# Optimization experiments

Hardware: AMD Instinct MI355X
Metric: run time of the kernel (lower is better)

The kernel has to match this reference:

```python
import jax, jax.numpy as jnp
import numpy as np

NUM_HEADS = 6
HEAD_SIZE = 64
N_EMBD = 384


def setup_inputs() -> dict:
    key = jax.random.key(0)
    ks = jax.random.split(key, 6)
    B, T, C = 4, 2048, N_EMBD
    D = NUM_HEADS * HEAD_SIZE  # 384
    x = jax.random.normal(ks[0], (B, T, C), dtype=jnp.float32)
    scale = 1.0 / np.sqrt(C)
    Wq = jax.random.normal(ks[1], (C, D), dtype=jnp.float32) * scale
    Wk = jax.random.normal(ks[2], (C, D), dtype=jnp.float32) * scale
    Wv = jax.random.normal(ks[3], (C, D), dtype=jnp.float32) * scale
    Wp = jax.random.normal(ks[4], (D, N_EMBD), dtype=jnp.float32) * scale
    bp = jnp.zeros((N_EMBD,), dtype=jnp.float32)
    return {"x": x, "Wq": Wq, "Wk": Wk, "Wv": Wv, "Wp": Wp, "bp": bp}


def reference(x, Wq, Wk, Wv, Wp, bp):
    B, T, C = x.shape
    H, Dh = NUM_HEADS, HEAD_SIZE
    # QKV projections (no bias), split into heads: [B, H, T, Dh]
    q = (x @ Wq).reshape(B, T, H, Dh).transpose(0, 2, 1, 3)
    k = (x @ Wk).reshape(B, T, H, Dh).transpose(0, 2, 1, 3)
    v = (x @ Wv).reshape(B, T, H, Dh).transpose(0, 2, 1, 3)
    # scaled dot-product scores [B, H, T, T]
    scores = jnp.einsum("bhqd,bhkd->bhqk", q, k) / jnp.sqrt(jnp.float32(Dh))
    causal = jnp.tril(jnp.ones((T, T), dtype=bool))
    scores = jnp.where(causal, scores, jnp.float32(-1e9))
    attn = jax.nn.softmax(scores, axis=-1)
    # dropout is identity at inference (Keras Dropout inactive outside training)
    out = jnp.einsum("bhqk,bhkd->bhqd", attn, v)
    out = out.transpose(0, 2, 1, 3).reshape(B, T, H * Dh)
    return out @ Wp + bp
```

## Files before the change

kernel.cpp:

```cpp
#include <hip/hip_runtime.h>
#include <hip/hip_bf16.h>

typedef __bf16 bf16x8 __attribute__((ext_vector_type(8)));
typedef float floatx4 __attribute__((ext_vector_type(4)));
typedef unsigned short us4 __attribute__((ext_vector_type(4)));
typedef unsigned short us8 __attribute__((ext_vector_type(8)));
typedef unsigned short ushort_t;

#define MFMA(a,b,c) __builtin_amdgcn_mfma_f32_16x16x32_bf16((a),(b),(c),0,0,0)


__device__ __forceinline__ ushort_t f2bf(float f){
  unsigned u = __builtin_bit_cast(unsigned, f);
  u = u + 0x7fffu + ((u>>16)&1u);
  return (ushort_t)(u>>16);
}

__device__ __forceinline__ us4 pack4(float4 a){
  us4 o;
  o[0]=f2bf(a.x); o[1]=f2bf(a.y); o[2]=f2bf(a.z); o[3]=f2bf(a.w);
  return o;
}

__device__ __forceinline__ us4 cvt4(floatx4 v){
  union { us4 s; __hip_bfloat162 h[2]; } u;
  float2 t;
  t.x=v[0]; t.y=v[1]; u.h[0]=__float22bfloat162_rn(t);
  t.x=v[2]; t.y=v[3]; u.h[1]=__float22bfloat162_rn(t);
  return u.s;
}

__global__ __launch_bounds__(256) void prep(
    const float* __restrict__ x,
    const float* __restrict__ w0, const float* __restrict__ w1,
    const float* __restrict__ w2, const float* __restrict__ w3,
    ushort_t* __restrict__ xb,
    ushort_t* __restrict__ wt_qkv, ushort_t* __restrict__ wt_p){
  __shared__ ushort_t tile[64][65];
  int bx = blockIdx.x;
  if (bx < 3072){
    int i = (bx*256 + threadIdx.x)*4;
    int row = i/384, col = i - row*384;
    float4 v = *(const float4*)(x + i);
    us4 o;
    o[0]=f2bf(v.x); o[1]=f2bf(v.y); o[2]=f2bf(v.z); o[3]=f2bf(v.w);
    *(us4*)(xb + ((row>>4)*48 + (col>>3))*128 + (row&15)*8 + (col&7)) = o;
    return;
  }
  int t6 = bx - 3072;
  int z = t6/36, rem = t6%36, by = rem/6, bxx = rem%6;
  const float* src; ushort_t* dst;
  if      (z==0){ src=w0; dst=wt_qkv;             }
  else if (z==1){ src=w1; dst=wt_qkv + 147456;    }
  else if (z==2){ src=w2; dst=wt_qkv + 2*147456;  }
  else          { src=w3; dst=wt_p;               }
  int r0 = by*64, c0 = bxx*64;
  int t = threadIdx.x, r = t>>2, cs = (t&3)*16;
  #pragma unroll
  for (int i=0;i<16;i++) tile[r][cs+i] = f2bf(src[(r0+r)*384 + c0+cs+i]);
  __syncthreads();
  int n = c0 + r, t16n = n>>4, rn = n&15;
  int k0 = r0 + cs;
  #pragma unroll
  for (int i=0;i<16;i++){
    int k = k0 + i;
    dst[(t16n*48 + (k>>3))*128 + rn*8 + (k&7)] = tile[cs+i][r];
  }
}

__global__ __launch_bounds__(64) void qkv_gemm(
    const ushort_t* __restrict__ x, const ushort_t* __restrict__ wt,
    ushort_t* __restrict__ qb, ushort_t* __restrict__ kb, ushort_t* __restrict__ vtb){
  int lane = threadIdx.x&63, l15 = lane&15, quad = lane>>4;
  int mb = blockIdx.x*64, mt = blockIdx.x*4;
  int z  = blockIdx.y/6;
  int nt16 = (blockIdx.y - z*6)*4;
  int n0 = nt16*16;
  const ushort_t* wbase = wt + z*147456;
  floatx4 acc[4][4];
  #pragma unroll
  for (int qs=0;qs<4;qs++)
    #pragma unroll
    for (int nt=0;nt<4;nt++) acc[qs][nt]=(floatx4){0,0,0,0};
  #pragma unroll
  for (int kt=0; kt<12; kt++){
    bf16x8 a[4], b[4];
    #pragma unroll
    for (int qs=0; qs<4; qs++)
      a[qs] = *(const bf16x8*)(x + ((mt+qs)*48 + kt*4+quad)*128 + l15*8);
    #pragma unroll
    for (int nt=0; nt<4; nt++)
      b[nt] = *(const bf16x8*)(wbase + ((nt16+nt)*48 + kt*4+quad)*128 + l15*8);
    #pragma unroll
    for (int qs=0; qs<4; qs++)
      #pragma unroll
      for (int nt=0; nt<4; nt++)
        acc[qs][nt] = MFMA(a[qs], b[nt], acc[qs][nt]);
  }
  int h = n0>>6;
  if (z == 2){
    #pragma unroll
    for (int qs=0; qs<4; qs++){
      int rbase = mb + qs*16 + quad*4;
      int b_ = rbase >> 11, rr = rbase & 2047;
      int ct = rr>>3, e0 = rr&7;
      #pragma unroll
      for (int nt=0; nt<4; nt++){
        float4 v; v.x=acc[qs][nt][0]; v.y=acc[qs][nt][1];
                  v.z=acc[qs][nt][2]; v.w=acc[qs][nt][3];
        *(us4*)(vtb + ((b_*6+h)*1024 + nt*256 + ct)*128 + l15*8 + e0) = pack4(v);
      }
    }
  } else {
    #pragma unroll
    for (int qs=0; qs<4; qs++){
      int rbase = mb + qs*16 + quad*4;
      int b_ = rbase>>11, rr = rbase&2047;
      int t16 = rr>>4, rlo = rr&15;
      #pragma unroll
      for (int nt=0; nt<4; nt++){
        int hc = nt*16 + l15;
        int base = ((b_*6+h)*1024 + t16*8 + (hc>>3))*128 + (hc&7);
        #pragma unroll
        for (int j=0; j<4; j++){
          float val = acc[qs][nt][j];
          if (z==0) val *= 0.18033688011112042f;
          ushort_t hv = f2bf(val);
          if (z==0) qb[base + (rlo+j)*8] = hv;
          else      kb[base + (rlo+j)*8] = hv;
        }
      }
    }
  }
}

__device__ __forceinline__ void subtile(
    const bf16x8 (&kf)[4][2], const bf16x8 (&vf)[4][2], bf16x8 ones,
    bf16x8 qf0, bf16x8 qf1,
    floatx4 (&o4)[4], floatx4& lsum,
    ushort_t* pwv, int qg, int kv0, bool diag, int l15, int quad){
  floatx4 s[4];
  #pragma unroll
  for (int nt=0; nt<4; nt++){
    floatx4 z = {0,0,0,0};
    z = MFMA(kf[nt][0], qf0, z);
    z = MFMA(kf[nt][1], qf1, z);
    s[nt] = z;
  }
  ushort_t* prow = pwv + l15*72;
  if (diag){
    #pragma unroll
    for (int nt=0; nt<4; nt++){
      floatx4 p;
      #pragma unroll
      for (int r=0;r<4;r++){
        int kvg = kv0 + nt*16 + quad*4 + r;
        float sv = (kvg > qg) ? -1e30f : s[nt][r];
        p[r] = exp2f(sv);
      }
      *(us4*)(prow + nt*16 + quad*4) = cvt4(p);
    }
  } else {
    #pragma unroll
    for (int nt=0; nt<4; nt++){
      floatx4 p;
      #pragma unroll
      for (int r=0;r<4;r++) p[r] = exp2f(s[nt][r]);
      *(us4*)(prow + nt*16 + quad*4) = cvt4(p);
    }
  }
  bf16x8 pa0 = *(const bf16x8*)(prow + quad*8);
  bf16x8 pa1 = *(const bf16x8*)(prow + 32 + quad*8);
  #pragma unroll
  for (int nt=0; nt<4; nt++){
    o4[nt] = MFMA(pa0, vf[nt][0], o4[nt]);
    o4[nt] = MFMA(pa1, vf[nt][1], o4[nt]);
  }
  lsum = MFMA(pa0, ones, lsum);
  lsum = MFMA(pa1, ones, lsum);
}

__global__ __launch_bounds__(256,2) void attn(
    const ushort_t* __restrict__ qb, const ushort_t* __restrict__ kb,
    const ushort_t* __restrict__ vtb, ushort_t* __restrict__ ob){
  __shared__ float smem[4608];
  int bx = blockIdx.x;
  int hb = bx % 24;
  int qi = bx / 24;
  int qt = 31 - qi;
  int h = hb % 6, b = hb / 6;
  int lane = threadIdx.x&63, w = threadIdx.x>>6, l15 = lane&15, quad = lane>>4;
  int q0 = qt*64;
  const ushort_t* qbase = qb  + (b*6+h)*131072;
  const ushort_t* kbase = kb  + (b*6+h)*131072;
  const ushort_t* vbase = vtb + (b*6+h)*131072;

  bf16x8 qf[4][2];
  #pragma unroll
  for (int qs=0; qs<4; qs++){
    const ushort_t* qp = qbase + ((qt*4+qs)*8 + quad)*128 + l15*8;
    qf[qs][0] = *(const bf16x8*)(qp);
    qf[qs][1] = *(const bf16x8*)(qp + 512);
  }
  union { us8 u; bf16x8 v; } onesu;
  #pragma unroll
  for (int i=0;i<8;i++) onesu.u[i] = 0x3F80;
  bf16x8 ones = onesu.v;

  floatx4 o[4][4];
  floatx4 lsum[4];
  #pragma unroll
  for (int qs=0;qs<4;qs++){
    lsum[qs] = (floatx4){0,0,0,0};
    #pragma unroll
    for (int i=0;i<4;i++) o[qs][i]=(floatx4){0,0,0,0};
  }

  ushort_t* pw = (ushort_t*)smem + w*1152;

  for (int kt=w; kt<=qt; kt+=4){
    int kv0 = kt*64;
    bf16x8 kf[4][2], vf[4][2];
    #pragma unroll
    for (int nt=0; nt<4; nt++){
      const ushort_t* kp = kbase + ((kt*4+nt)*8 + quad)*128 + l15*8;
      kf[nt][0] = *(const bf16x8*)(kp);
      kf[nt][1] = *(const bf16x8*)(kp + 512);
      const ushort_t* vp = vbase + (nt*256 + kt*8 + quad)*128 + l15*8;
      vf[nt][0] = *(const bf16x8*)(vp);
      vf[nt][1] = *(const bf16x8*)(vp + 512);
    }
    bool diag = (kt == qt);
    subtile(kf,vf,ones,qf[0][0],qf[0][1], o[0], lsum[0], pw, q0   +l15, kv0, diag, l15, quad);
    subtile(kf,vf,ones,qf[1][0],qf[1][1], o[1], lsum[1], pw, q0+16+l15, kv0, diag, l15, quad);
    subtile(kf,vf,ones,qf[2][0],qf[2][1], o[2], lsum[2], pw, q0+32+l15, kv0, diag, l15, quad);
    subtile(kf,vf,ones,qf[3][0],qf[3][1], o[3], lsum[3], pw, q0+48+l15, kv0, diag, l15, quad);
  }

  float* lsh = smem + 4352;
  if (l15==0){
    #pragma unroll
    for (int qs=0;qs<4;qs++)
      #pragma unroll
      for (int j=0;j<4;j++)
        lsh[w*64 + qs*16 + quad*4 + j] = lsum[qs][j];
  }

  #pragma unroll
  for (int qs=0; qs<4; qs++){
    __syncthreads();
    #pragma unroll
    for (int j=0;j<4;j++){
      int r16 = quad*4 + j;
      #pragma unroll
      for (int nt=0;nt<4;nt++)
        smem[w*1088 + r16*68 + nt*16 + l15] = o[qs][nt][j];
    }
    __syncthreads();
    #pragma unroll
    for (int jj=0;jj<4;jj++){
      int r16 = w*4 + jj;
      float l = lsh[qs*16+r16] + lsh[64+qs*16+r16]
              + lsh[128+qs*16+r16] + lsh[192+qs*16+r16];
      float acc = smem[r16*68+lane] + smem[1088 + r16*68+lane]
                + smem[2176 + r16*68+lane] + smem[3264 + r16*68+lane];
      ob[((b*128 + qt*4 + qs)*48 + h*8 + (lane>>3))*128 + r16*8 + (lane&7)]
          = f2bf(acc/l);
    }
  }
}

__global__ __launch_bounds__(64) void proj_gemm(
    const ushort_t* __restrict__ a, const ushort_t* __restrict__ wpt,
    const float* __restrict__ bp, float* __restrict__ out){
  int lane = threadIdx.x&63, l15 = lane&15, quad = lane>>4;
  int mb = blockIdx.x*64, mt = blockIdx.x*4;
  int nb = blockIdx.y*64, nt16 = blockIdx.y*4;
  floatx4 acc[4][4];
  #pragma unroll
  for (int qs=0;qs<4;qs++)
    #pragma unroll
    for (int nt=0;nt<4;nt++) acc[qs][nt]=(floatx4){0,0,0,0};
  #pragma unroll
  for (int kt=0; kt<12; kt++){
    bf16x8 av[4], bv[4];
    #pragma unroll
    for (int qs=0; qs<4; qs++)
      av[qs] = *(const bf16x8*)(a + ((mt+qs)*48 + kt*4+quad)*128 + l15*8);
    #pragma unroll
    for (int nt=0; nt<4; nt++)
      bv[nt] = *(const bf16x8*)(wpt + ((nt16+nt)*48 + kt*4+quad)*128 + l15*8);
    #pragma unroll
    for (int qs=0; qs<4; qs++)
      #pragma unroll
      for (int nt=0; nt<4; nt++)
        acc[qs][nt] = MFMA(av[qs], bv[nt], acc[qs][nt]);
  }
  #pragma unroll
  for (int qs=0; qs<4; qs++){
    #pragma unroll
    for (int nt=0; nt<4; nt++){
      int c = nb + nt*16 + l15;
      float bias = bp[c];
      #pragma unroll
      for (int j=0; j<4; j++){
        int r = mb + qs*16 + quad*4 + j;
        out[r*384 + c] = acc[qs][nt][j] + bias;
      }
    }
  }
}

extern "C" void kernel_launch(void* const* d_in, const int* in_sizes, int n_in,
                              void* d_out, int out_size, void* d_ws, size_t ws_size,
                              hipStream_t stream){
  const float* x  = (const float*)d_in[0];
  const float* Wq = (const float*)d_in[1];
  const float* Wk = (const float*)d_in[2];
  const float* Wv = (const float*)d_in[3];
  const float* Wp = (const float*)d_in[4];
  const float* bp = (const float*)d_in[5];
  float* out = (float*)d_out;

  ushort_t* xb  = (ushort_t*)d_ws;
  ushort_t* wt  = xb  + 8192*384;
  ushort_t* wpt = wt  + 1152*384;
  ushort_t* qb  = wpt + 384*384;
  ushort_t* kb  = qb  + 8192*384;
  ushort_t* vtb = kb  + 8192*384;
  ushort_t* ab  = vtb + 8192*384;

  prep     <<<dim3(3216),   256, 0, stream>>>(x,Wq,Wk,Wv,Wp,xb,wt,wpt);
  qkv_gemm <<<dim3(128,18), 64,  0, stream>>>(xb, wt, qb, kb, vtb);
  attn     <<<dim3(768),    256, 0, stream>>>(qb, kb, vtb, ab);
  proj_gemm<<<dim3(128,6),  64,  0, stream>>>(ab, wpt, bp, out);
}
```

Baseline: 137.1 us.

## Pair short and long 32-row query tiles per attention block for causal load balance

```diff
diff --git a/kernel.cpp b/kernel.cpp
--- a/kernel.cpp
+++ b/kernel.cpp
@@ -186,39 +186,44 @@
   __shared__ float smem[4608];
   int bx = blockIdx.x;
   int hb = bx % 24;
-  int qi = bx / 24;
-  int qt = 31 - qi;
+  int p  = bx / 24;
+  int tA = p, tB = 63 - p;
+  int ktA = tA >> 1, ktB = tB >> 1;
   int h = hb % 6, b = hb / 6;
   int lane = threadIdx.x&63, w = threadIdx.x>>6, l15 = lane&15, quad = lane>>4;
-  int q0 = qt*64;
   const ushort_t* qbase = qb  + (b*6+h)*131072;
   const ushort_t* kbase = kb  + (b*6+h)*131072;
   const ushort_t* vbase = vtb + (b*6+h)*131072;
 
-  bf16x8 qf[4][2];
-  #pragma unroll
-  for (int qs=0; qs<4; qs++){
-    const ushort_t* qp = qbase + ((qt*4+qs)*8 + quad)*128 + l15*8;
-    qf[qs][0] = *(const bf16x8*)(qp);
-    qf[qs][1] = *(const bf16x8*)(qp + 512);
+  bf16x8 qfA[2][2], qfB[2][2];
+  #pragma unroll
+  for (int s=0; s<2; s++){
+    const ushort_t* qpA = qbase + ((tA*2+s)*8 + quad)*128 + l15*8;
+    qfA[s][0] = *(const bf16x8*)(qpA);
+    qfA[s][1] = *(const bf16x8*)(qpA + 512);
+    const ushort_t* qpB = qbase + ((tB*2+s)*8 + quad)*128 + l15*8;
+    qfB[s][0] = *(const bf16x8*)(qpB);
+    qfB[s][1] = *(const bf16x8*)(qpB + 512);
   }
   union { us8 u; bf16x8 v; } onesu;
   #pragma unroll
   for (int i=0;i<8;i++) onesu.u[i] = 0x3F80;
   bf16x8 ones = onesu.v;
 
-  floatx4 o[4][4];
-  floatx4 lsum[4];
-  #pragma unroll
-  for (int qs=0;qs<4;qs++){
-    lsum[qs] = (floatx4){0,0,0,0};
-    #pragma unroll
-    for (int i=0;i<4;i++) o[qs][i]=(floatx4){0,0,0,0};
+  floatx4 oA[2][4], oB[2][4];
+  floatx4 lsA[2], lsB[2];
+  #pragma unroll
+  for (int s=0;s<2;s++){
+    lsA[s] = (floatx4){0,0,0,0};
+    lsB[s] = (floatx4){0,0,0,0};
+    #pragma unroll
+    for (int i=0;i<4;i++){ oA[s][i]=(floatx4){0,0,0,0}; oB[s][i]=(floatx4){0,0,0,0}; }
   }
 
   ushort_t* pw = (ushort_t*)smem + w*1152;
-
-  for (int kt=w; kt<=qt; kt+=4){
+  int qA0 = tA*32, qB0 = tB*32;
+
+  for (int kt=w; kt<=ktB; kt+=4){
     int kv0 = kt*64;
     bf16x8 kf[4][2], vf[4][2];
     #pragma unroll
@@ -230,44 +235,52 @@
       vf[nt][0] = *(const bf16x8*)(vp);
       vf[nt][1] = *(const bf16x8*)(vp + 512);
     }
-    bool diag = (kt == qt);
-    subtile(kf,vf,ones,qf[0][0],qf[0][1], o[0], lsum[0], pw, q0   +l15, kv0, diag, l15, quad);
-    subtile(kf,vf,ones,qf[1][0],qf[1][1], o[1], lsum[1], pw, q0+16+l15, kv0, diag, l15, quad);
-    subtile(kf,vf,ones,qf[2][0],qf[2][1], o[2], lsum[2], pw, q0+32+l15, kv0, diag, l15, quad);
-    subtile(kf,vf,ones,qf[3][0],qf[3][1], o[3], lsum[3], pw, q0+48+l15, kv0, diag, l15, quad);
+    bool diagB = (kt == ktB);
+    subtile(kf,vf,ones,qfB[0][0],qfB[0][1], oB[0], lsB[0], pw, qB0   +l15, kv0, diagB, l15, quad);
+    subtile(kf,vf,ones,qfB[1][0],qfB[1][1], oB[1], lsB[1], pw, qB0+16+l15, kv0, diagB, l15, quad);
+    if (kt <= ktA){
+      bool diagA = (kt == ktA);
+      subtile(kf,vf,ones,qfA[0][0],qfA[0][1], oA[0], lsA[0], pw, qA0   +l15, kv0, diagA, l15, quad);
+      subtile(kf,vf,ones,qfA[1][0],qfA[1][1], oA[1], lsA[1], pw, qA0+16+l15, kv0, diagA, l15, quad);
+    }
   }
 
   float* lsh = smem + 4352;
   if (l15==0){
     #pragma unroll
-    for (int qs=0;qs<4;qs++)
-      #pragma unroll
-      for (int j=0;j<4;j++)
-        lsh[w*64 + qs*16 + quad*4 + j] = lsum[qs][j];
-  }
-
-  #pragma unroll
-  for (int qs=0; qs<4; qs++){
+    for (int j=0;j<4;j++){
+      lsh[w*64 +      quad*4 + j] = lsA[0][j];
+      lsh[w*64 + 16 + quad*4 + j] = lsA[1][j];
+      lsh[w*64 + 32 + quad*4 + j] = lsB[0][j];
+      lsh[w*64 + 48 + quad*4 + j] = lsB[1][j];
+    }
+  }
+
+  auto do_chunk = [&](const floatx4 (&oc)[4], int c, int grc){
     __syncthreads();
     #pragma unroll
     for (int j=0;j<4;j++){
       int r16 = quad*4 + j;
       #pragma unroll
       for (int nt=0;nt<4;nt++)
-        smem[w*1088 + r16*68 + nt*16 + l15] = o[qs][nt][j];
+        smem[w*1088 + r16*68 + nt*16 + l15] = oc[nt][j];
     }
     __syncthreads();
     #pragma unroll
     for (int jj=0;jj<4;jj++){
       int r16 = w*4 + jj;
-      float l = lsh[qs*16+r16] + lsh[64+qs*16+r16]
-              + lsh[128+qs*16+r16] + lsh[192+qs*16+r16];
+      float l = lsh[c*16+r16] + lsh[64+c*16+r16]
+              + lsh[128+c*16+r16] + lsh[192+c*16+r16];
       float acc = smem[r16*68+lane] + smem[1088 + r16*68+lane]
                 + smem[2176 + r16*68+lane] + smem[3264 + r16*68+lane];
-      ob[((b*128 + qt*4 + qs)*48 + h*8 + (lane>>3))*128 + r16*8 + (lane&7)]
+      ob[((b*128 + grc)*48 + h*8 + (lane>>3))*128 + r16*8 + (lane&7)]
           = f2bf(acc/l);
     }
-  }
+  };
+  do_chunk(oA[0], 0, tA*2);
+  do_chunk(oA[1], 1, tA*2+1);
+  do_chunk(oB[0], 2, tB*2);
+  do_chunk(oB[1], 3, tB*2+1);
 }
 
 __global__ __launch_bounds__(64) void proj_gemm(
```

After: 133.3 us. 2.7% less time.
